# Optimization experiments

Hardware: AMD Instinct MI355X
Metric: run time of the kernel (lower is better)

## Reference

```python
import jax, jax.numpy as jnp
import numpy as np

N_BINS = 10  # init default of ECELoss


def setup_inputs() -> dict:
    key = jax.random.key(0)
    k1, k2 = jax.random.split(key)
    N, C = 2_000_000, 100
    raw = jax.random.normal(k1, (N, C), dtype=jnp.float32)
    # module computes exp(logits) and expects confidences in (0, 1],
    # so the logits it receives are log-probabilities
    logits = jax.nn.log_softmax(raw, axis=1)
    labels = jax.random.randint(k2, (N,), 0, C, dtype=jnp.int64)
    return {"logits": logits, "labels": labels}


def reference(logits, labels):
    softmaxes = jnp.exp(logits)                       # [N, C]
    confidences = jnp.max(softmaxes, axis=1)          # [N]
    predictions = jnp.argmax(softmaxes, axis=1)       # [N]
    accuracies = (predictions == labels).astype(jnp.float32)

    n = confidences.shape[0]
    # bin i holds conf in (i/n_bins, (i+1)/n_bins]  ->  ceil(conf*n_bins)-1
    bin_idx = jnp.ceil(confidences * N_BINS).astype(jnp.int32) - 1
    # conf <= 0 belongs to no bin (strict lower bound on bin 0); conf > 1
    # already maps to an out-of-range index. Out-of-range ids are dropped
    # by segment_sum.
    bin_idx = jnp.where(confidences <= 0.0, N_BINS, bin_idx)

    ones = jnp.ones_like(confidences)
    counts = jax.ops.segment_sum(ones, bin_idx, num_segments=N_BINS)
    sum_conf = jax.ops.segment_sum(confidences, bin_idx, num_segments=N_BINS)
    sum_acc = jax.ops.segment_sum(accuracies, bin_idx, num_segments=N_BINS)

    prop_in_bin = counts / n
    safe = jnp.maximum(counts, 1.0)
    gap = jnp.abs(sum_conf / safe - sum_acc / safe)
    ece = jnp.sum(jnp.where(counts > 0, gap * prop_in_bin, 0.0))
    return ece.reshape(1)
```

## Files before the change

kernel.cpp:

```cpp
#include <hip/hip_runtime.h>
#include <math.h>

#define NBINS 10
#define BLOCKS 768
#define THREADS 128
#define TILE_ROWS 64
#define ROW_F4 25
#define TILE_F4 (TILE_ROWS * ROW_F4)
#define LOADS_PER_LANE 25


__global__ void ece_zero_ws(float* ws) {
    int i = threadIdx.x;
    if (i < 3 * NBINS) ws[i] = 0.0f;
}

__global__ __launch_bounds__(THREADS) void ece_main(
        const float* __restrict__ logits,
        const int* __restrict__ labels,
        float* __restrict__ ws,
        int N) {
    __shared__ __align__(16) float tile[2][TILE_ROWS * 100];
    __shared__ float sbin[3 * NBINS];
    const int tid = threadIdx.x;
    if (tid < 3 * NBINS) sbin[tid] = 0.0f;
    __syncthreads();

    const int lane = tid & 63;
    const int w = tid >> 6;
    float* const mybuf = &tile[w][0];

    const long long nTiles = ((long long)N + TILE_ROWS - 1) / TILE_ROWS;
    const long long waveId = (long long)blockIdx.x * 2 + w;
    const long long nWaves = (long long)gridDim.x * 2;

    const float4* const lg4 = (const float4*)logits;
    const long long lastF4 = (long long)N * ROW_F4 - 1;

    typedef const __attribute__((address_space(1))) void* gptr_t;
    typedef __attribute__((address_space(3))) void* lptr_t;

    for (long long t = waveId; t < nTiles; t += nWaves) {
        const long long base_f4 = t * (long long)TILE_F4;

        asm volatile("s_waitcnt lgkmcnt(0)" ::: "memory");

        #pragma unroll
        for (int j = 0; j < LOADS_PER_LANE; ++j) {
            long long g = base_f4 + j * 64 + lane;
            if (g > lastF4) g = lastF4;
            __builtin_amdgcn_global_load_lds(
                (gptr_t)(lg4 + g),
                (lptr_t)(mybuf + j * 256),
                16, 0, 0);
        }
        asm volatile("s_waitcnt vmcnt(0)" ::: "memory");

        const long long row = t * TILE_ROWS + lane;
        if (row < (long long)N) {
            const float4* const rp = (const float4*)(mybuf + lane * 100);
            float m = -INFINITY;
            int midx = 0;
            #pragma unroll
            for (int j = 0; j < ROW_F4; ++j) {
                const float4 v = rp[j];
                const int e = 4 * j;
                if (v.x > m) { m = v.x; midx = e; }
                if (v.y > m) { m = v.y; midx = e + 1; }
                if (v.z > m) { m = v.z; midx = e + 2; }
                if (v.w > m) { m = v.w; midx = e + 3; }
            }
            const float conf = expf(m);
            const int b = (int)ceilf(conf * 10.0f) - 1;
            const float acc = (midx == labels[row]) ? 1.0f : 0.0f;
            if (b >= 0 && b < NBINS) {
                atomicAdd(&sbin[b], 1.0f);
                atomicAdd(&sbin[NBINS + b], conf);
                atomicAdd(&sbin[2 * NBINS + b], acc);
            }
        }
    }

    __syncthreads();
    if (tid < 3 * NBINS) {
        const float s = sbin[tid];
        if (s != 0.0f) atomicAdd(&ws[tid], s);
    }
}

__global__ void ece_final(const float* __restrict__ ws, float* __restrict__ out, int N) {
    if (threadIdx.x == 0 && blockIdx.x == 0) {
        float ece = 0.0f;
        for (int b = 0; b < NBINS; ++b) {
            const float cnt = ws[b];
            if (cnt > 0.0f) {
                const float avg_conf = ws[NBINS + b] / cnt;
                const float avg_acc  = ws[2 * NBINS + b] / cnt;
                ece += fabsf(avg_conf - avg_acc) * (cnt / (float)N);
            }
        }
        out[0] = ece;
    }
}

extern "C" void kernel_launch(void* const* d_in, const int* in_sizes, int n_in,
                              void* d_out, int out_size, void* d_ws, size_t ws_size,
                              hipStream_t stream) {
    const float* logits = (const float*)d_in[0];
    const int*   labels = (const int*)d_in[1];
    float* out = (float*)d_out;
    float* ws  = (float*)d_ws;

    const int N = in_sizes[1];

    ece_zero_ws<<<1, 64, 0, stream>>>(ws);
    ece_main<<<BLOCKS, THREADS, 0, stream>>>(logits, labels, ws, N);
    ece_final<<<1, 64, 0, stream>>>(ws, out, N);
}
```

Baseline: 993.9 us.

## Double-buffer LDS tile loads per wave and fuse final ECE reduction

Each block becomes a single wave that owns two LDS buffers. The next tile's global-to-LDS loads are issued before the current tile is processed, with a partial vmcnt wait, so memory latency overlaps the argmax compute. The separate final kernel is removed: a last-block-done counter in the workspace lets the final block compute ECE, which saves one launch. In exchange the grid has half as many waves (768 single-wave blocks), and the prefetch beyond the end is clamped to the last element, which adds redundant loads. There is also no LDS wait or barrier before overwriting a buffer, and sbin is zeroed with no barrier, so wave-level ordering is relied upon.

```diff
diff --git a/kernel.cpp b/kernel.cpp
--- a/kernel.cpp
+++ b/kernel.cpp
@@ -3,103 +3,116 @@
 
 #define NBINS 10
 #define BLOCKS 768
-#define THREADS 128
+#define THREADS 64
 #define TILE_ROWS 64
 #define ROW_F4 25
 #define TILE_F4 (TILE_ROWS * ROW_F4)
-#define LOADS_PER_LANE 25
+#define LPL 25
 
+
+typedef const __attribute__((address_space(1))) void* gptr_t;
+typedef __attribute__((address_space(3))) void* lptr_t;
 
 __global__ void ece_zero_ws(float* ws) {
     int i = threadIdx.x;
-    if (i < 3 * NBINS) ws[i] = 0.0f;
+    if (i < 3 * NBINS + 1) ws[i] = 0.0f;
 }
 
 __global__ __launch_bounds__(THREADS) void ece_main(
         const float* __restrict__ logits,
         const int* __restrict__ labels,
         float* __restrict__ ws,
+        float* __restrict__ out,
         int N) {
-    __shared__ __align__(16) float tile[2][TILE_ROWS * 100];
+    __shared__ __align__(16) float bufA[TILE_ROWS * 100];
+    __shared__ __align__(16) float bufB[TILE_ROWS * 100];
     __shared__ float sbin[3 * NBINS];
-    const int tid = threadIdx.x;
-    if (tid < 3 * NBINS) sbin[tid] = 0.0f;
-    __syncthreads();
 
-    const int lane = tid & 63;
-    const int w = tid >> 6;
-    float* const mybuf = &tile[w][0];
+    const int lane = threadIdx.x;
+    if (lane < 3 * NBINS) sbin[lane] = 0.0f;
 
     const long long nTiles = ((long long)N + TILE_ROWS - 1) / TILE_ROWS;
-    const long long waveId = (long long)blockIdx.x * 2 + w;
-    const long long nWaves = (long long)gridDim.x * 2;
+    const long long waveId = blockIdx.x;
+    const long long nWaves = gridDim.x;
 
     const float4* const lg4 = (const float4*)logits;
     const long long lastF4 = (long long)N * ROW_F4 - 1;
 
-    typedef const __attribute__((address_space(1))) void* gptr_t;
-    typedef __attribute__((address_space(3))) void* lptr_t;
+    float* pa = bufA;
+    float* pb = bufB;
 
-    for (long long t = waveId; t < nTiles; t += nWaves) {
-        const long long base_f4 = t * (long long)TILE_F4;
+    long long t = waveId;
+    if (t < nTiles) {
+        {
+            const long long base = t * (long long)TILE_F4;
+            #pragma unroll
+            for (int j = 0; j < LPL; ++j) {
+                long long g = base + j * 64 + lane;
+                if (g > lastF4) g = lastF4;
+                __builtin_amdgcn_global_load_lds((gptr_t)(lg4 + g),
+                                                 (lptr_t)(pa + j * 256), 16, 0, 0);
+            }
+        }
+        for (; t < nTiles; t += nWaves) {
+            {
+                const long long base = (t + nWaves) * (long long)TILE_F4;
+                #pragma unroll
+                for (int j = 0; j < LPL; ++j) {
+                    long long g = base + j * 64 + lane;
+                    if (g > lastF4) g = lastF4;
+                    __builtin_amdgcn_global_load_lds((gptr_t)(lg4 + g),
+                                                     (lptr_t)(pb + j * 256), 16, 0, 0);
+                }
+            }
+            asm volatile("s_waitcnt vmcnt(25)" ::: "memory");
 
-        asm volatile("s_waitcnt lgkmcnt(0)" ::: "memory");
-
-        #pragma unroll
-        for (int j = 0; j < LOADS_PER_LANE; ++j) {
-            long long g = base_f4 + j * 64 + lane;
-            if (g > lastF4) g = lastF4;
-            __builtin_amdgcn_global_load_lds(
-                (gptr_t)(lg4 + g),
-                (lptr_t)(mybuf + j * 256),
-                16, 0, 0);
-        }
-        asm volatile("s_waitcnt vmcnt(0)" ::: "memory");
-
-        const long long row = t * TILE_ROWS + lane;
-        if (row < (long long)N) {
-            const float4* const rp = (const float4*)(mybuf + lane * 100);
-            float m = -INFINITY;
-            int midx = 0;
-            #pragma unroll
-            for (int j = 0; j < ROW_F4; ++j) {
-                const float4 v = rp[j];
-                const int e = 4 * j;
-                if (v.x > m) { m = v.x; midx = e; }
-                if (v.y > m) { m = v.y; midx = e + 1; }
-                if (v.z > m) { m = v.z; midx = e + 2; }
-                if (v.w > m) { m = v.w; midx = e + 3; }
+            const long long row = t * TILE_ROWS + lane;
+            if (row < (long long)N) {
+                const float4* const rp = (const float4*)(pa + lane * 100);
+                float m = -INFINITY;
+                int midx = 0;
+                #pragma unroll
+                for (int j = 0; j < ROW_F4; ++j) {
+                    const float4 v = rp[j];
+                    const int e = 4 * j;
+                    if (v.x > m) { m = v.x; midx = e; }
+                    if (v.y > m) { m = v.y; midx = e + 1; }
+                    if (v.z > m) { m = v.z; midx = e + 2; }
+                    if (v.w > m) { m = v.w; midx = e + 3; }
+                }
+                const float conf = expf(m);
+                const int b = (int)ceilf(conf * 10.0f) - 1;
+                const float acc = (midx == labels[row]) ? 1.0f : 0.0f;
+                if (b >= 0 && b < NBINS) {
+                    atomicAdd(&sbin[b], 1.0f);
+                    atomicAdd(&sbin[NBINS + b], conf);
+                    atomicAdd(&sbin[2 * NBINS + b], acc);
+                }
             }
-            const float conf = expf(m);
-            const int b = (int)ceilf(conf * 10.0f) - 1;
-            const float acc = (midx == labels[row]) ? 1.0f : 0.0f;
-            if (b >= 0 && b < NBINS) {
-                atomicAdd(&sbin[b], 1.0f);
-                atomicAdd(&sbin[NBINS + b], conf);
-                atomicAdd(&sbin[2 * NBINS + b], acc);
-            }
+            float* tmp = pa; pa = pb; pb = tmp;
         }
     }
 
-    __syncthreads();
-    if (tid < 3 * NBINS) {
-        const float s = sbin[tid];
-        if (s != 0.0f) atomicAdd(&ws[tid], s);
+    if (lane < 3 * NBINS) {
+        const float s = sbin[lane];
+        if (s != 0.0f) atomicAdd(&ws[lane], s);
     }
-}
-
-__global__ void ece_final(const float* __restrict__ ws, float* __restrict__ out, int N) {
-    if (threadIdx.x == 0 && blockIdx.x == 0) {
-        float ece = 0.0f;
-        for (int b = 0; b < NBINS; ++b) {
-            const float cnt = ws[b];
-            if (cnt > 0.0f) {
-                const float avg_conf = ws[NBINS + b] / cnt;
-                const float avg_acc  = ws[2 * NBINS + b] / cnt;
-                ece += fabsf(avg_conf - avg_acc) * (cnt / (float)N);
+    __threadfence();
+    if (lane == 0) {
+        const unsigned int old = atomicAdd((unsigned int*)(ws + 30), 1u);
+        if (old == gridDim.x - 1) {
+            __threadfence();
+            float ece = 0.0f;
+            for (int b = 0; b < NBINS; ++b) {
+                const float cnt = atomicAdd(&ws[b], 0.0f);
+                if (cnt > 0.0f) {
+                    const float avg_conf = atomicAdd(&ws[NBINS + b], 0.0f) / cnt;
+                    const float avg_acc  = atomicAdd(&ws[2 * NBINS + b], 0.0f) / cnt;
+                    ece += fabsf(avg_conf - avg_acc) * (cnt / (float)N);
+                }
             }
+            out[0] = ece;
         }
-        out[0] = ece;
     }
 }
 
@@ -114,6 +127,5 @@
     const int N = in_sizes[1];
 
     ece_zero_ws<<<1, 64, 0, stream>>>(ws);
-    ece_main<<<BLOCKS, THREADS, 0, stream>>>(logits, labels, ws, N);
-    ece_final<<<1, 64, 0, stream>>>(ws, out, N);
+    ece_main<<<BLOCKS, THREADS, 0, stream>>>(logits, labels, ws, out, N);
 }
```

New measurement: 1.029 ms. +3.5%, slower.
